# Kernel tuning notes

Hardware: AMD Instinct MI355X
Metric: run time of the kernel (lower is better)

## Reference

```python
import jax, jax.numpy as jnp
import numpy as np

# Scalar quantization params (QLinear __init__ args)
FEATURE_BITWIDTH = 8
WEIGHT_BITWIDTH = 8
INPUT_ZERO_POINT = -3
OUTPUT_ZERO_POINT = -5
INPUT_SCALE = 0.05
OUTPUT_SCALE = 0.1
QMIN = -(1 << (FEATURE_BITWIDTH - 1))   # -128
QMAX = (1 << (FEATURE_BITWIDTH - 1)) - 1  # 127

M, K, N = 8192, 4096, 4096


def float_to_fixed_point(x, bitwidth):
    """Represent x (0 < x < 1) as int_scale * 2^-frac_bits with int_scale
    in [2^(bitwidth-2), 2^(bitwidth-1)) (mantissa fits in signed `bitwidth` bits)."""
    frac_bits = (bitwidth - 1 - jnp.ceil(jnp.log2(x))).astype(jnp.int32)
    int_scale = jnp.round(x * jnp.exp2(frac_bits.astype(jnp.float32))).astype(jnp.int32)
    return int_scale, frac_bits


def setup_inputs() -> dict:
    key = jax.random.key(0)
    k1, k2, k3, k4 = jax.random.split(key, 4)
    qinput = jax.random.randint(k1, (M, K), -128, 128, dtype=jnp.int8)
    qweight = jax.random.randint(k2, (N, K), -128, 128, dtype=jnp.int8)
    qbias = jax.random.randint(k3, (N,), -(1 << 16), 1 << 16, dtype=jnp.int32)
    # per-output-channel weight scale; keeps folded scale in (0, 1)
    weight_scale = jax.random.uniform(k4, (N,), jnp.float32, 0.002, 0.02)
    return {"qinput": qinput, "qweight": qweight, "qbias": qbias,
            "weight_scale": weight_scale}


def reference(qinput, qweight, qbias, weight_scale):
    w32 = qweight.astype(jnp.int32)                      # [N, K]
    # Qbias' = qbias - sum_k(qweight) * Zin  (bias shift folding input zero point)
    shifted_qbias = qbias - w32.sum(axis=1) * INPUT_ZERO_POINT  # [N]
    # int32 GEMM: [M, K] @ [K, N] + bias
    acc = qinput.astype(jnp.int32) @ w32.T + shifted_qbias[None, :]  # [M, N]
    # fixed-point requantization: (acc * int_scale) >> frac_bits + Zout
    folded_scale = INPUT_SCALE * weight_scale / OUTPUT_SCALE         # [N], in (0,1)
    int_scale, frac_bits = float_to_fixed_point(folded_scale, FEATURE_BITWIDTH)
    # widen to int64 for the multiply so the (acc * int_scale) product cannot wrap
    prod = acc.astype(jnp.int64) * int_scale.astype(jnp.int64)[None, :]
    scaled = jnp.right_shift(prod, frac_bits.astype(jnp.int64)[None, :])  # arithmetic >>
    out = scaled + OUTPUT_ZERO_POINT
    return jnp.clip(out, QMIN, QMAX).astype(jnp.int8)
```

## Files before the change

### kernel.cpp

```cpp
#include <hip/hip_runtime.h>
#include <cstdint>
#include <cstddef>

#define M_DIM 8192
#define N_DIM 4096
#define K_DIM 4096

#define BM 128
#define BN 128
#define BK 128

typedef int int32x4 __attribute__((ext_vector_type(4)));


typedef __attribute__((address_space(1))) const void* gas_cptr;
typedef __attribute__((address_space(3))) void* las_ptr;

__device__ __forceinline__ void async_copy16(const void* g, void* l) {
    __builtin_amdgcn_global_load_lds((gas_cptr)g, (las_ptr)l, 16, 0, 0);
}

__device__ __forceinline__ int32x4 pack16(const int* p) {
    const int32x4* v = (const int32x4*)p;
    int32x4 w0 = v[0], w1 = v[1], w2 = v[2], w3 = v[3];
    int32x4 r;
    r.x = (w0.x & 0xFF) | ((w0.y & 0xFF) << 8) | ((w0.z & 0xFF) << 16) | (w0.w << 24);
    r.y = (w1.x & 0xFF) | ((w1.y & 0xFF) << 8) | ((w1.z & 0xFF) << 16) | (w1.w << 24);
    r.z = (w2.x & 0xFF) | ((w2.y & 0xFF) << 8) | ((w2.z & 0xFF) << 16) | (w2.w << 24);
    r.w = (w3.x & 0xFF) | ((w3.y & 0xFF) << 8) | ((w3.z & 0xFF) << 16) | (w3.w << 24);
    return r;
}

__global__ void ql_detect_kernel(const int* a, const int* b, int* ws) {
    int t = threadIdx.x;
    int fa = 0, fb = 0;
    for (int i = t; i < 4096; i += 64) {
        int va = a[i]; if (va > 127 || va < -128) fa = 1;
        int vb = b[i]; if (vb > 127 || vb < -128) fb = 1;
    }
    unsigned long long ba = __ballot(fa);
    unsigned long long bb = __ballot(fb);
    if (t == 0) { ws[0] = ba ? 1 : 0; ws[1] = bb ? 1 : 0; }
}

__global__ __launch_bounds__(256)
void ql_pack2_kernel(const void* asrc, const void* bsrc, int* adst, int* bdst,
                     const int* ws, long ndwA, long ndwW) {
    const int fa = __builtin_amdgcn_readfirstlane(ws[0]);
    const int fb = __builtin_amdgcn_readfirstlane(ws[1]);
    const long total = ndwA + ndwW;
    const long stride = (long)gridDim.x * 256;
    for (long c = (long)blockIdx.x * 256 + threadIdx.x; c < total; c += stride) {
        if (c < ndwA) {
            if (fa) adst[c] = ((const int*)asrc)[c];
            else {
                int32x4 v = ((const int32x4*)asrc)[c];
                adst[c] = (v.x & 0xFF) | ((v.y & 0xFF) << 8) | ((v.z & 0xFF) << 16) | (v.w << 24);
            }
        } else {
            long d = c - ndwA;
            if (fb) bdst[d] = ((const int*)bsrc)[d];
            else {
                int32x4 v = ((const int32x4*)bsrc)[d];
                bdst[d] = (v.x & 0xFF) | ((v.y & 0xFF) << 8) | ((v.z & 0xFF) << 16) | (v.w << 24);
            }
        }
    }
}

__global__ void ql_prep8_kernel(const int8_t* w8, const int* qbias,
                                const float* wscale, int* ws) {
    const int lane = threadIdx.x & 63;
    const int wid  = threadIdx.x >> 6;
    const int n = blockIdx.x * 4 + wid;

    const int32x4* row = (const int32x4*)(w8 + (size_t)n * K_DIM);
    int s = 0;
    for (int c = lane; c < K_DIM / 16; c += 64) {
        int32x4 v = row[c];
#pragma unroll
        for (int j = 0; j < 4; ++j) {
            int w = (j == 0) ? v.x : (j == 1) ? v.y : (j == 2) ? v.z : v.w;
            s += (int)(int8_t)(w) + (int)(int8_t)(w >> 8)
               + (int)(int8_t)(w >> 16) + (w >> 24);
        }
    }
#pragma unroll
    for (int off = 32; off > 0; off >>= 1) s += __shfl_down(s, off, 64);

    if (lane == 0) {
        ws[16 + n] = qbias[n] + 3 * s;
        float folded = (0.05f * wscale[n]) / 0.1f;
        int fbits = (int)(7.0f - ceilf(log2f(folded)));
        int isc = (int)rintf(folded * exp2f((float)fbits));
        ws[16 + N_DIM + n] = isc;
        ws[16 + 2 * N_DIM + n] = fbits;
    }
}

__global__ void ql_prep_kernel(const void* wptr, const int* qbias,
                               const float* wscale, int* ws) {
    const int lane = threadIdx.x & 63;
    const int wid  = threadIdx.x >> 6;
    const int n = blockIdx.x * 4 + wid;
    const int b8 = __builtin_amdgcn_readfirstlane(ws[1]);

    int s = 0;
    if (b8) {
        const int32x4* row = (const int32x4*)((const int8_t*)wptr + (size_t)n * K_DIM);
        for (int c = lane; c < K_DIM / 16; c += 64) {
            int32x4 v = row[c];
#pragma unroll
            for (int j = 0; j < 4; ++j) {
                int w = (j == 0) ? v.x : (j == 1) ? v.y : (j == 2) ? v.z : v.w;
                s += (int)(int8_t)(w) + (int)(int8_t)(w >> 8)
                   + (int)(int8_t)(w >> 16) + (w >> 24);
            }
        }
    } else {
        const int32x4* row = (const int32x4*)((const int*)wptr + (size_t)n * K_DIM);
        for (int c = lane; c < K_DIM / 4; c += 64) {
            int32x4 v = row[c];
            s += v.x + v.y + v.z + v.w;
        }
    }
#pragma unroll
    for (int off = 32; off > 0; off >>= 1) s += __shfl_down(s, off, 64);

    if (lane == 0) {
        ws[16 + n] = qbias[n] + 3 * s;
        float folded = (0.05f * wscale[n]) / 0.1f;
        int fbits = (int)(7.0f - ceilf(log2f(folded)));
        int isc = (int)rintf(folded * exp2f((float)fbits));
        ws[16 + N_DIM + n] = isc;
        ws[16 + 2 * N_DIM + n] = fbits;
    }
}

__device__ __forceinline__ int acc_elem(const int32x4& a, int r) {
    return (r == 0) ? a.x : (r == 1) ? a.y : (r == 2) ? a.z : a.w;
}

__global__ __launch_bounds__(256)
void ql_gemm_kernel(const int8_t* aptr, const int8_t* bptr, const int* ws, int* out) {
    __shared__ int32x4 Ab[2][BM * BK / 16];
    __shared__ int32x4 Bb[2][BN * BK / 16];

    const int t    = threadIdx.x;
    const int lane = t & 63;
    const int wid  = t >> 6;
    const int bn = blockIdx.x;
    const int bm = blockIdx.y;

    const int wm = (wid >> 1) * 64;
    const int wn = (wid & 1) * 64;
    const int qm = lane & 15;
    const int qh = lane >> 4;

    int32x4 acc[4][4] = {};

#pragma unroll
    for (int r = 0; r < 4; ++r) {
        const int c    = r * 256 + t;
        const int row  = c >> 3;
        const int colg = (c & 7) ^ (row & 7);
        async_copy16(aptr + (size_t)(bm * BM + row) * K_DIM + colg * 16, &Ab[0][c]);
        async_copy16(bptr + (size_t)(bn * BN + row) * K_DIM + colg * 16, &Bb[0][c]);
    }

    int cur = 0;
    for (int kt = 0; kt < K_DIM / BK; ++kt) {
        __syncthreads();
        if (kt + 1 < K_DIM / BK) {
            const int k1 = (kt + 1) * BK;
            const int nxt = cur ^ 1;
#pragma unroll
            for (int r = 0; r < 4; ++r) {
                const int c    = r * 256 + t;
                const int row  = c >> 3;
                const int colg = (c & 7) ^ (row & 7);
                async_copy16(aptr + (size_t)(bm * BM + row) * K_DIM + k1 + colg * 16,
                             &Ab[nxt][c]);
                async_copy16(bptr + (size_t)(bn * BN + row) * K_DIM + k1 + colg * 16,
                             &Bb[nxt][c]);
            }
        }

#pragma unroll
        for (int s = 0; s < 2; ++s) {
            const int colk = s * 4 + qh;
            int32x4 af[4], bf[4];
#pragma unroll
            for (int i = 0; i < 4; ++i) {
                const int ra = wm + i * 16 + qm;
                const int rb = wn + i * 16 + qm;
                af[i] = Ab[cur][ra * 8 + (colk ^ (ra & 7))];
                bf[i] = Bb[cur][rb * 8 + (colk ^ (rb & 7))];
            }
#pragma unroll
            for (int i = 0; i < 4; ++i)
#pragma unroll
                for (int j = 0; j < 4; ++j)
                    acc[i][j] = __builtin_amdgcn_mfma_i32_16x16x64_i8(
                        af[i], bf[j], acc[i][j], 0, 0, 0);
        }
        cur ^= 1;
    }

    __syncthreads();
    const int* qb  = ws + 16;
    const int* isc = ws + 16 + N_DIM;
    const int* fbt = ws + 16 + 2 * N_DIM;

    int* sc  = (int*)&Ab[0][0];
    int* wsc = sc + wid * 1088;

#pragma unroll
    for (int i = 0; i < 4; ++i) {
#pragma unroll
        for (int j = 0; j < 4; ++j) {
            const int n_g = bn * BN + wn + j * 16 + qm;
            const int b0 = qb[n_g];
            const int s0 = isc[n_g];
            const int f0 = fbt[n_g];
#pragma unroll
            for (int r = 0; r < 4; ++r) {
                int v = acc_elem(acc[i][j], r) + b0;
                long long p = (long long)v * (long long)s0;
                int o = (int)(p >> f0) - 5;
                o = o < -128 ? -128 : (o > 127 ? 127 : o);
                wsc[(qh * 4 + r) * 68 + j * 16 + qm] = o;
            }
        }
#pragma unroll
        for (int p4 = 0; p4 < 4; ++p4) {
            const int lr = p4 * 4 + qh;
            int32x4 vv = *(const int32x4*)&wsc[lr * 68 + qm * 4];
            const size_t g = (size_t)(bm * BM + wm + i * 16 + lr) * N_DIM
                           + bn * BN + wn + qm * 4;
            *(int32x4*)(out + g) = vv;
        }
    }
}

__global__ __launch_bounds__(256)
void ql_gemm_fb_kernel(const void* aptr, const void* bptr, const int* ws, int* out) {
    __shared__ int32x4 Als[BM * BK / 16];
    __shared__ int32x4 Bls[BN * BK / 16];

    const int a8 = __builtin_amdgcn_readfirstlane(ws[0]);
    const int b8 = __builtin_amdgcn_readfirstlane(ws[1]);

    const int t    = threadIdx.x;
    const int lane = t & 63;
    const int wid  = t >> 6;
    const int bn = blockIdx.x;
    const int bm = blockIdx.y;

    const int wm = (wid >> 1) * 64;
    const int wn = (wid & 1) * 64;
    const int qm = lane & 15;
    const int qh = lane >> 4;

    int32x4 acc[4][4] = {};

    for (int kt = 0; kt < K_DIM / BK; ++kt) {
        __syncthreads();
        const int k0 = kt * BK;
#pragma unroll
        for (int r = 0; r < 4; ++r) {
            const int c    = r * 256 + t;
            const int row  = c >> 3;
            const int colg = (c & 7) ^ (row & 7);
            const size_t offA = (size_t)(bm * BM + row) * K_DIM + k0 + colg * 16;
            const size_t offB = (size_t)(bn * BN + row) * K_DIM + k0 + colg * 16;
            if (a8) async_copy16((const int8_t*)aptr + offA, &Als[c]);
            else    Als[c] = pack16((const int*)aptr + offA);
            if (b8) async_copy16((const int8_t*)bptr + offB, &Bls[c]);
            else    Bls[c] = pack16((const int*)bptr + offB);
        }
        __syncthreads();

#pragma unroll
        for (int s = 0; s < 2; ++s) {
            const int colk = s * 4 + qh;
            int32x4 af[4], bf[4];
#pragma unroll
            for (int i = 0; i < 4; ++i) {
                const int ra = wm + i * 16 + qm;
                const int rb = wn + i * 16 + qm;
                af[i] = Als[ra * 8 + (colk ^ (ra & 7))];
                bf[i] = Bls[rb * 8 + (colk ^ (rb & 7))];
            }
#pragma unroll
            for (int i = 0; i < 4; ++i)
#pragma unroll
                for (int j = 0; j < 4; ++j)
                    acc[i][j] = __builtin_amdgcn_mfma_i32_16x16x64_i8(
                        af[i], bf[j], acc[i][j], 0, 0, 0);
        }
    }

    const int* qb  = ws + 16;
    const int* isc = ws + 16 + N_DIM;
    const int* fbt = ws + 16 + 2 * N_DIM;
#pragma unroll
    for (int j = 0; j < 4; ++j) {
        const int n_g = bn * BN + wn + j * 16 + qm;
        const int b0 = qb[n_g];
        const int s0 = isc[n_g];
        const int f0 = fbt[n_g];
#pragma unroll
        for (int i = 0; i < 4; ++i) {
            const int m_base = bm * BM + wm + i * 16 + qh * 4;
#pragma unroll
            for (int r = 0; r < 4; ++r) {
                int v = acc_elem(acc[i][j], r) + b0;
                long long p = (long long)v * (long long)s0;
                int o = (int)(p >> f0) - 5;
                o = o < -128 ? -128 : (o > 127 ? 127 : o);
                out[(size_t)(m_base + r) * N_DIM + n_g] = o;
            }
        }
    }
}

extern "C" void kernel_launch(void* const* d_in, const int* in_sizes, int n_in,
                              void* d_out, int out_size, void* d_ws, size_t ws_size,
                              hipStream_t stream) {
    const void* qin    = d_in[0];
    const void* qwt    = d_in[1];
    const int* qbias   = (const int*)d_in[2];
    const float* wscal = (const float*)d_in[3];
    int* ws  = (int*)d_ws;
    int* out = (int*)d_out;

    hipLaunchKernelGGL(ql_detect_kernel, dim3(1), dim3(64), 0, stream,
                       (const int*)qin, (const int*)qwt, ws);

    const size_t need = 65536 + (size_t)M_DIM * K_DIM + (size_t)N_DIM * K_DIM;
    if (ws_size >= need) {
        int8_t* a8 = (int8_t*)d_ws + 65536;
        int8_t* w8 = a8 + (size_t)M_DIM * K_DIM;
        const long ndwA = (long)M_DIM * K_DIM / 4;
        const long ndwW = (long)N_DIM * K_DIM / 4;
        hipLaunchKernelGGL(ql_pack2_kernel, dim3((unsigned)((ndwA + ndwW) / (256 * 4))),
                           dim3(256), 0, stream,
                           qin, qwt, (int*)a8, (int*)w8, ws, ndwA, ndwW);
        hipLaunchKernelGGL(ql_prep8_kernel, dim3(N_DIM / 4), dim3(256), 0, stream,
                           w8, qbias, wscal, ws);
        hipLaunchKernelGGL(ql_gemm_kernel, dim3(N_DIM / BN, M_DIM / BM), dim3(256), 0, stream,
                           a8, w8, ws, out);
    } else {
        hipLaunchKernelGGL(ql_prep_kernel, dim3(N_DIM / 4), dim3(256), 0, stream,
                           qwt, qbias, wscal, ws);
        hipLaunchKernelGGL(ql_gemm_fb_kernel, dim3(N_DIM / BN, M_DIM / BM), dim3(256), 0, stream,
                           qin, qwt, ws, out);
    }
}
```

Baseline: 449.0 us.

## Fuse weight row-sum into pack kernel; single-buffer GEMM with direct epilogue

Computes the per-row weight sums inside the pack kernel through wave reductions and atomics, replacing the separate prep8 pass with a small finalize kernel and a memset. The GEMM drops its double-buffered async prefetch in favour of a single LDS buffer with load-then-sync each k-tile. The epilogue now writes scalar ints straight to global memory instead of staging through LDS for 16-byte stores. This saves one pass over the weights but removes the load/compute overlap and coalesced stores, so the main GEMM will likely be slower.

```diff
diff --git a/kernel.cpp b/kernel.cpp
--- a/kernel.cpp
+++ b/kernel.cpp
@@ -45,9 +45,10 @@
 
 __global__ __launch_bounds__(256)
 void ql_pack2_kernel(const void* asrc, const void* bsrc, int* adst, int* bdst,
-                     const int* ws, long ndwA, long ndwW) {
+                     int* ws, long ndwA, long ndwW) {
     const int fa = __builtin_amdgcn_readfirstlane(ws[0]);
     const int fb = __builtin_amdgcn_readfirstlane(ws[1]);
+    const int lane = threadIdx.x & 63;
     const long total = ndwA + ndwW;
     const long stride = (long)gridDim.x * 256;
     for (long c = (long)blockIdx.x * 256 + threadIdx.x; c < total; c += stride) {
@@ -59,30 +60,62 @@
             }
         } else {
             long d = c - ndwA;
-            if (fb) bdst[d] = ((const int*)bsrc)[d];
+            int w;
+            if (fb) w = ((const int*)bsrc)[d];
             else {
                 int32x4 v = ((const int32x4*)bsrc)[d];
-                bdst[d] = (v.x & 0xFF) | ((v.y & 0xFF) << 8) | ((v.z & 0xFF) << 16) | (v.w << 24);
-            }
-        }
-    }
-}
-
-__global__ void ql_prep8_kernel(const int8_t* w8, const int* qbias,
-                                const float* wscale, int* ws) {
+                w = (v.x & 0xFF) | ((v.y & 0xFF) << 8) | ((v.z & 0xFF) << 16) | (v.w << 24);
+            }
+            bdst[d] = w;
+            int s = (int)(int8_t)(w) + (int)(int8_t)(w >> 8)
+                  + (int)(int8_t)(w >> 16) + (w >> 24);
+#pragma unroll
+            for (int off = 32; off > 0; off >>= 1) s += __shfl_down(s, off, 64);
+            if (lane == 0) {
+                const int n = (int)(d >> 10);
+                atomicAdd(&ws[16 + n], s);
+            }
+        }
+    }
+}
+
+__global__ __launch_bounds__(256)
+void ql_finalize_kernel(const int* qbias, const float* wscale, int* ws) {
+    const int n = blockIdx.x * 256 + threadIdx.x;
+    if (n >= N_DIM) return;
+    const int s = ws[16 + n];
+    ws[16 + n] = qbias[n] + 3 * s;
+    float folded = (0.05f * wscale[n]) / 0.1f;
+    int fbits = (int)(7.0f - ceilf(log2f(folded)));
+    int isc = (int)rintf(folded * exp2f((float)fbits));
+    ws[16 + N_DIM + n] = isc;
+    ws[16 + 2 * N_DIM + n] = fbits;
+}
+
+__global__ void ql_prep_kernel(const void* wptr, const int* qbias,
+                               const float* wscale, int* ws) {
     const int lane = threadIdx.x & 63;
     const int wid  = threadIdx.x >> 6;
     const int n = blockIdx.x * 4 + wid;
-
-    const int32x4* row = (const int32x4*)(w8 + (size_t)n * K_DIM);
+    const int b8 = __builtin_amdgcn_readfirstlane(ws[1]);
+
     int s = 0;
-    for (int c = lane; c < K_DIM / 16; c += 64) {
-        int32x4 v = row[c];
-#pragma unroll
-        for (int j = 0; j < 4; ++j) {
-            int w = (j == 0) ? v.x : (j == 1) ? v.y : (j == 2) ? v.z : v.w;
-            s += (int)(int8_t)(w) + (int)(int8_t)(w >> 8)
-               + (int)(int8_t)(w >> 16) + (w >> 24);
+    if (b8) {
+        const int32x4* row = (const int32x4*)((const int8_t*)wptr + (size_t)n * K_DIM);
+        for (int c = lane; c < K_DIM / 16; c += 64) {
+            int32x4 v = row[c];
+#pragma unroll
+            for (int j = 0; j < 4; ++j) {
+                int w = (j == 0) ? v.x : (j == 1) ? v.y : (j == 2) ? v.z : v.w;
+                s += (int)(int8_t)(w) + (int)(int8_t)(w >> 8)
+                   + (int)(int8_t)(w >> 16) + (w >> 24);
+            }
+        }
+    } else {
+        const int32x4* row = (const int32x4*)((const int*)wptr + (size_t)n * K_DIM);
+        for (int c = lane; c < K_DIM / 4; c += 64) {
+            int32x4 v = row[c];
+            s += v.x + v.y + v.z + v.w;
         }
     }
 #pragma unroll
@@ -98,53 +131,14 @@
     }
 }
 
-__global__ void ql_prep_kernel(const void* wptr, const int* qbias,
-                               const float* wscale, int* ws) {
-    const int lane = threadIdx.x & 63;
-    const int wid  = threadIdx.x >> 6;
-    const int n = blockIdx.x * 4 + wid;
-    const int b8 = __builtin_amdgcn_readfirstlane(ws[1]);
-
-    int s = 0;
-    if (b8) {
-        const int32x4* row = (const int32x4*)((const int8_t*)wptr + (size_t)n * K_DIM);
-        for (int c = lane; c < K_DIM / 16; c += 64) {
-            int32x4 v = row[c];
-#pragma unroll
-            for (int j = 0; j < 4; ++j) {
-                int w = (j == 0) ? v.x : (j == 1) ? v.y : (j == 2) ? v.z : v.w;
-                s += (int)(int8_t)(w) + (int)(int8_t)(w >> 8)
-                   + (int)(int8_t)(w >> 16) + (w >> 24);
-            }
-        }
-    } else {
-        const int32x4* row = (const int32x4*)((const int*)wptr + (size_t)n * K_DIM);
-        for (int c = lane; c < K_DIM / 4; c += 64) {
-            int32x4 v = row[c];
-            s += v.x + v.y + v.z + v.w;
-        }
-    }
-#pragma unroll
-    for (int off = 32; off > 0; off >>= 1) s += __shfl_down(s, off, 64);
-
-    if (lane == 0) {
-        ws[16 + n] = qbias[n] + 3 * s;
-        float folded = (0.05f * wscale[n]) / 0.1f;
-        int fbits = (int)(7.0f - ceilf(log2f(folded)));
-        int isc = (int)rintf(folded * exp2f((float)fbits));
-        ws[16 + N_DIM + n] = isc;
-        ws[16 + 2 * N_DIM + n] = fbits;
-    }
-}
-
 __device__ __forceinline__ int acc_elem(const int32x4& a, int r) {
     return (r == 0) ? a.x : (r == 1) ? a.y : (r == 2) ? a.z : a.w;
 }
 
 __global__ __launch_bounds__(256)
 void ql_gemm_kernel(const int8_t* aptr, const int8_t* bptr, const int* ws, int* out) {
-    __shared__ int32x4 Ab[2][BM * BK / 16];
-    __shared__ int32x4 Bb[2][BN * BK / 16];
+    __shared__ int32x4 Als[BM * BK / 16];
+    __shared__ int32x4 Bls[BN * BK / 16];
 
     const int t    = threadIdx.x;
     const int lane = t & 63;
@@ -159,32 +153,20 @@
 
     int32x4 acc[4][4] = {};
 
-#pragma unroll
-    for (int r = 0; r < 4; ++r) {
-        const int c    = r * 256 + t;
-        const int row  = c >> 3;
-        const int colg = (c & 7) ^ (row & 7);
-        async_copy16(aptr + (size_t)(bm * BM + row) * K_DIM + colg * 16, &Ab[0][c]);
-        async_copy16(bptr + (size_t)(bn * BN + row) * K_DIM + colg * 16, &Bb[0][c]);
-    }
-
-    int cur = 0;
     for (int kt = 0; kt < K_DIM / BK; ++kt) {
         __syncthreads();
-        if (kt + 1 < K_DIM / BK) {
-            const int k1 = (kt + 1) * BK;
-            const int nxt = cur ^ 1;
-#pragma unroll
-            for (int r = 0; r < 4; ++r) {
-                const int c    = r * 256 + t;
-                const int row  = c >> 3;
-                const int colg = (c & 7) ^ (row & 7);
-                async_copy16(aptr + (size_t)(bm * BM + row) * K_DIM + k1 + colg * 16,
-                             &Ab[nxt][c]);
-                async_copy16(bptr + (size_t)(bn * BN + row) * K_DIM + k1 + colg * 16,
-                             &Bb[nxt][c]);
-            }
-        }
+        const int k0 = kt * BK;
+#pragma unroll
+        for (int r = 0; r < 4; ++r) {
+            const int c    = r * 256 + t;
+            const int row  = c >> 3;
+            const int colg = (c & 7) ^ (row & 7);
+            const size_t offA = (size_t)(bm * BM + row) * K_DIM + k0 + colg * 16;
+            const size_t offB = (size_t)(bn * BN + row) * K_DIM + k0 + colg * 16;
+            async_copy16(aptr + offA, &Als[c]);
+            async_copy16(bptr + offB, &Bls[c]);
+        }
+        __syncthreads();
 
 #pragma unroll
         for (int s = 0; s < 2; ++s) {
@@ -194,8 +176,8 @@
             for (int i = 0; i < 4; ++i) {
                 const int ra = wm + i * 16 + qm;
                 const int rb = wn + i * 16 + qm;
-                af[i] = Ab[cur][ra * 8 + (colk ^ (ra & 7))];
-                bf[i] = Bb[cur][rb * 8 + (colk ^ (rb & 7))];
+                af[i] = Als[ra * 8 + (colk ^ (ra & 7))];
+                bf[i] = Bls[rb * 8 + (colk ^ (rb & 7))];
             }
 #pragma unroll
             for (int i = 0; i < 4; ++i)
@@ -204,41 +186,28 @@
                     acc[i][j] = __builtin_amdgcn_mfma_i32_16x16x64_i8(
                         af[i], bf[j], acc[i][j], 0, 0, 0);
         }
-        cur ^= 1;
-    }
-
-    __syncthreads();
+    }
+
     const int* qb  = ws + 16;
     const int* isc = ws + 16 + N_DIM;
     const int* fbt = ws + 16 + 2 * N_DIM;
-
-    int* sc  = (int*)&Ab[0][0];
-    int* wsc = sc + wid * 1088;
-
-#pragma unroll
-    for (int i = 0; i < 4; ++i) {
-#pragma unroll
-        for (int j = 0; j < 4; ++j) {
-            const int n_g = bn * BN + wn + j * 16 + qm;
-            const int b0 = qb[n_g];
-            const int s0 = isc[n_g];
-            const int f0 = fbt[n_g];
+#pragma unroll
+    for (int j = 0; j < 4; ++j) {
+        const int n_g = bn * BN + wn + j * 16 + qm;
+        const int b0 = qb[n_g];
+        const int s0 = isc[n_g];
+        const int f0 = fbt[n_g];
+#pragma unroll
+        for (int i = 0; i < 4; ++i) {
+            const int m_base = bm * BM + wm + i * 16 + qh * 4;
 #pragma unroll
             for (int r = 0; r < 4; ++r) {
                 int v = acc_elem(acc[i][j], r) + b0;
                 long long p = (long long)v * (long long)s0;
                 int o = (int)(p >> f0) - 5;
                 o = o < -128 ? -128 : (o > 127 ? 127 : o);
-                wsc[(qh * 4 + r) * 68 + j * 16 + qm] = o;
-            }
-        }
-#pragma unroll
-        for (int p4 = 0; p4 < 4; ++p4) {
-            const int lr = p4 * 4 + qh;
-            int32x4 vv = *(const int32x4*)&wsc[lr * 68 + qm * 4];
-            const size_t g = (size_t)(bm * BM + wm + i * 16 + lr) * N_DIM
-                           + bn * BN + wn + qm * 4;
-            *(int32x4*)(out + g) = vv;
+                out[(size_t)(m_base + r) * N_DIM + n_g] = o;
+            }
         }
     }
 }
@@ -344,11 +313,12 @@
         int8_t* w8 = a8 + (size_t)M_DIM * K_DIM;
         const long ndwA = (long)M_DIM * K_DIM / 4;
         const long ndwW = (long)N_DIM * K_DIM / 4;
+        hipMemsetAsync(ws + 16, 0, N_DIM * sizeof(int), stream);
         hipLaunchKernelGGL(ql_pack2_kernel, dim3((unsigned)((ndwA + ndwW) / (256 * 4))),
                            dim3(256), 0, stream,
                            qin, qwt, (int*)a8, (int*)w8, ws, ndwA, ndwW);
-        hipLaunchKernelGGL(ql_prep8_kernel, dim3(N_DIM / 4), dim3(256), 0, stream,
-                           w8, qbias, wscal, ws);
+        hipLaunchKernelGGL(ql_finalize_kernel, dim3((N_DIM + 255) / 256), dim3(256),
+                           0, stream, qbias, wscal, ws);
         hipLaunchKernelGGL(ql_gemm_kernel, dim3(N_DIM / BN, M_DIM / BM), dim3(256), 0, stream,
                            a8, w8, ws, out);
     } else {
```

New measurement: 447.5 us. Within noise of the previous version (-0.3%).
